# Performance work log

Hardware: AMD Instinct MI355X
Metric: run time of the kernel (lower is better)

Reference implementation:

```python
import jax, jax.numpy as jnp
import numpy as np

N, E, G = 50000, 800000, 128          # nodes, edges, graphs
L, T, F = 4, 4, 20                    # conv layers, towers, per-tower width
D = T * F                             # 80 = hidden dim
EDGE_DIM = 16
AVG_DEG_LOG = float(np.log(17.0))     # avg_deg['log'] for avg in-degree ~16
EPS_STD = 1e-5
EPS_BN = 1e-5


def setup_inputs() -> dict:
    ks = iter(jax.random.split(jax.random.key(0), 32))
    rn = lambda *s: jax.random.normal(next(ks), s, jnp.float32) * 0.1
    return dict(
        x=jax.random.randint(next(ks), (N, 9), 0, 16),
        edge_index=jax.random.randint(next(ks), (2, E), 0, N),
        batch=jnp.sort(jax.random.randint(next(ks), (N,), 0, G)),
        edge_attr=rn(E, EDGE_DIM),
        atom_emb=rn(9, 16, D),
        edge_w=rn(L, EDGE_DIM, F), edge_b=jnp.zeros((L, F), jnp.float32),
        pre_w1=rn(L, T, 3 * F, F), pre_b1=jnp.zeros((L, T, F), jnp.float32),
        pre_w2=rn(L, T, F, F), pre_b2=jnp.zeros((L, T, F), jnp.float32),
        post_w1=rn(L, T, 13 * F, F), post_b1=jnp.zeros((L, T, F), jnp.float32),
        post_w2=rn(L, T, F, F), post_b2=jnp.zeros((L, T, F), jnp.float32),
        lin_w=rn(L, D, D), lin_b=jnp.zeros((L, D), jnp.float32),
        bn_g=jnp.ones((L, D), jnp.float32), bn_b=jnp.zeros((L, D), jnp.float32),
        mlp_w1=rn(D, 40), mlp_b1=jnp.zeros(40, jnp.float32),
        mlp_w2=rn(40, 20), mlp_b2=jnp.zeros(20, jnp.float32),
        mlp_w3=rn(20, 1), mlp_b3=jnp.zeros(1, jnp.float32),
    )


def _net(x, edge_index, batch, edge_attr, atom_emb, edge_w, edge_b, pre_w1,
         pre_b1, pre_w2, pre_b2, post_w1, post_b1, post_w2, post_b2, lin_w,
         lin_b, bn_g, bn_b, mlp_w1, mlp_b1, mlp_w2, mlp_b2, mlp_w3, mlp_b3):
    src, dst = edge_index[0], edge_index[1]
    # AtomEncoder: sum of 9 categorical embeddings -> [N, D]
    h = atom_emb[jnp.arange(9)[None, :], x].sum(1)
    deg_raw = jax.ops.segment_sum(jnp.ones((E,), jnp.float32), dst, N)
    deg = jnp.clip(deg_raw, 1.0)
    has_edge = (deg_raw > 0)[:, None, None]
    d3 = deg[:, None, None]
    logd = jnp.log(deg + 1.0)[:, None, None]
    for l in range(L):  # 4 PNAConv + BN + ReLU + residual (dropout off / eval)
        xt = h.reshape(N, T, F)
        ea = edge_attr @ edge_w[l] + edge_b[l]                      # [E, F]
        # message: concat(x_i, x_j, edge) -> per-tower pre MLP
        m = jnp.concatenate([xt[dst], xt[src],
                             jnp.broadcast_to(ea[:, None, :], (E, T, F))], -1)
        m = jax.nn.relu(jnp.einsum('eti,tio->eto', m, pre_w1[l]) + pre_b1[l])
        m = jnp.einsum('eti,tio->eto', m, pre_w2[l]) + pre_b2[l]    # [E,T,F]
        # multi-aggregator scatter-reduce
        mean = jax.ops.segment_sum(m, dst, N) / d3
        msq = jax.ops.segment_sum(m * m, dst, N) / d3
        std = jnp.sqrt(jax.nn.relu(msq - mean * mean) + EPS_STD)
        mn = jnp.where(has_edge, jax.ops.segment_min(m, dst, N), 0.0)
        mx = jnp.where(has_edge, jax.ops.segment_max(m, dst, N), 0.0)
        agg = jnp.concatenate([mean, mn, mx, std], -1)              # [N,T,4F]
        # degree scalers: identity, amplification, attenuation
        out = jnp.concatenate([agg, agg * (logd / AVG_DEG_LOG),
                               agg * (AVG_DEG_LOG / logd)], -1)     # [N,T,12F]
        out = jnp.concatenate([xt, out], -1)                        # [N,T,13F]
        out = jax.nn.relu(jnp.einsum('nti,tio->nto', out, post_w1[l]) + post_b1[l])
        out = jnp.einsum('nti,tio->nto', out, post_w2[l]) + post_b2[l]
        out = out.reshape(N, D) @ lin_w[l] + lin_b[l]
        # BatchNorm over nodes (batch statistics)
        mu = out.mean(0)
        var = jnp.mean((out - mu) ** 2, axis=0)
        out = (out - mu) * (bn_g[l] / jnp.sqrt(var + EPS_BN)) + bn_b[l]
        h = jax.nn.relu(out) + h
    # global mean pool over graphs + readout MLP
    cnt = jnp.clip(jax.ops.segment_sum(jnp.ones((N,), jnp.float32), batch, G), 1.0)
    g = jax.ops.segment_sum(h, batch, G) / cnt[:, None]
    g = jax.nn.relu(g @ mlp_w1 + mlp_b1)
    g = jax.nn.relu(g @ mlp_w2 + mlp_b2)
    return g @ mlp_w3 + mlp_b3                                      # [G, 1]


def reference(x, edge_index, batch, edge_attr, atom_emb, edge_w, edge_b, pre_w1,
              pre_b1, pre_w2, pre_b2, post_w1, post_b1, post_w2, post_b2, lin_w,
              lin_b, bn_g, bn_b, mlp_w1, mlp_b1, mlp_w2, mlp_b2, mlp_w3, mlp_b3):
    return _net(x, edge_index, batch, edge_attr, atom_emb, edge_w, edge_b, pre_w1,
                pre_b1, pre_w2, pre_b2, post_w1, post_b1, post_w2, post_b2,
                lin_w, lin_b, bn_g, bn_b, mlp_w1, mlp_b1, mlp_w2, mlp_b2,
                mlp_w3, mlp_b3)
```

## Files before the change

### kernel.cpp

```cpp
#include <hip/hip_runtime.h>
#include <hip/hip_bf16.h>

#define NN 50000
#define EE 800000
#define GG 128
#define LL 4
#define TT 4
#define FF 20
#define DD 80
#define SCAN_B ((NN + 1023) / 1024)
static constexpr float AVG_LOG = 2.8332133440562162f;

__device__ __forceinline__ float bf2f(unsigned short u) {
  return __uint_as_float((unsigned)u << 16);
}
__device__ __forceinline__ unsigned short f2bf(float f) {
  __hip_bfloat16 b = __float2bfloat16(f);
  return *(unsigned short*)&b;
}

__global__ __launch_bounds__(256) void k_h(const int* __restrict__ x,
                                           const float* __restrict__ atom_emb,
                                           float* __restrict__ h) {
  int idx = blockIdx.x * 256 + threadIdx.x;
  if (idx >= NN * DD) return;
  int n = idx / DD, d = idx - n * DD;
  const int* xr = x + n * 9;
  float acc = 0.f;
#pragma unroll
  for (int i = 0; i < 9; ++i) {
    int v = xr[i];
    acc += atom_emb[(i * 16 + v) * DD + d];
  }
  h[idx] = acc;
}

__global__ __launch_bounds__(256) void k_deg(const int* __restrict__ ei, int* __restrict__ cnt) {
  int e = blockIdx.x * 256 + threadIdx.x;
  if (e >= EE) return;
  atomicAdd(&cnt[ei[EE + e]], 1);
}

__global__ __launch_bounds__(1024) void k_scan_sum(const int* __restrict__ cnt, int* __restrict__ bsum) {
  __shared__ int red[1024];
  int tid = threadIdx.x;
  int i = blockIdx.x * 1024 + tid;
  red[tid] = (i < NN) ? cnt[i] : 0;
  __syncthreads();
  for (int off = 512; off > 0; off >>= 1) {
    if (tid < off) red[tid] += red[tid + off];
    __syncthreads();
  }
  if (tid == 0) bsum[blockIdx.x] = red[0];
}

__global__ void k_scan_top(const int* __restrict__ bsum, int* __restrict__ boff,
                           int* __restrict__ row_ptr) {
  if (threadIdx.x == 0 && blockIdx.x == 0) {
    int acc = 0;
    for (int b = 0; b < SCAN_B; ++b) { boff[b] = acc; acc += bsum[b]; }
    row_ptr[NN] = acc;
  }
}

__global__ __launch_bounds__(1024) void k_scan_apply(const int* __restrict__ cnt,
                                                     const int* __restrict__ boff,
                                                     int* __restrict__ row_ptr,
                                                     int* __restrict__ cursor) {
  __shared__ int sm[1024];
  int tid = threadIdx.x;
  int i = blockIdx.x * 1024 + tid;
  int v = (i < NN) ? cnt[i] : 0;
  sm[tid] = v;
  __syncthreads();
  for (int off = 1; off < 1024; off <<= 1) {
    int t = (tid >= off) ? sm[tid - off] : 0;
    __syncthreads();
    sm[tid] += t;
    __syncthreads();
  }
  int excl = boff[blockIdx.x] + sm[tid] - v;
  if (i < NN) { row_ptr[i] = excl; cursor[i] = excl; }
}

__global__ __launch_bounds__(256) void k_csrfill(const int* __restrict__ ei,
                                                 int* __restrict__ cursor,
                                                 int2* __restrict__ csr2,
                                                 int* __restrict__ csr_dst) {
  int e = blockIdx.x * 256 + threadIdx.x;
  if (e >= EE) return;
  int dst = ei[EE + e];
  int slot = atomicAdd(&cursor[dst], 1);
  csr2[slot] = make_int2(ei[e], e);
  csr_dst[slot] = dst;
}

__global__ __launch_bounds__(256) void k_nodeparams(const int* __restrict__ cnt,
                                                    float* __restrict__ inv_deg,
                                                    float* __restrict__ s1a,
                                                    float* __restrict__ s2a) {
  int n = blockIdx.x * 256 + threadIdx.x;
  if (n >= NN) return;
  int c = cnt[n];
  float deg = (c > 0) ? (float)c : 1.0f;
  inv_deg[n] = 1.0f / deg;
  float logd = logf(deg + 1.0f);
  s1a[n] = logd / AVG_LOG;
  s2a[n] = AVG_LOG / logd;
}

__global__ __launch_bounds__(64) void k_wcomb(const float* __restrict__ edge_w,
                                              const float* __restrict__ edge_b,
                                              const float* __restrict__ pre_w1,
                                              const float* __restrict__ pre_b1,
                                              float* __restrict__ wc,
                                              float* __restrict__ biasc, int l) {
  int t = blockIdx.x;
  int wt = l * TT + t;
  const float* W1 = pre_w1 + (size_t)wt * 1200;
  const float* ew = edge_w + (size_t)l * 16 * FF;
  const float* eb = edge_b + (size_t)l * FF;
  int j = threadIdx.x;
  if (j >= FF) return;
  for (int i = 0; i < 16; ++i) {
    float acc = 0.f;
#pragma unroll
    for (int f = 0; f < FF; ++f) acc = fmaf(ew[i * FF + f], W1[(40 + f) * FF + j], acc);
    wc[(t * 16 + i) * FF + j] = acc;
  }
  float b = pre_b1[wt * FF + j];
#pragma unroll
  for (int f = 0; f < FF; ++f) b = fmaf(eb[f], W1[(40 + f) * FF + j], b);
  biasc[t * FF + j] = b;
}

__global__ __launch_bounds__(256) void k_prenode(
    const float* __restrict__ h, const float* __restrict__ pre_w1,
    const float* __restrict__ biasc,
    unsigned short* __restrict__ predD, unsigned short* __restrict__ predS, int l) {
  int tid = threadIdx.x;
  int t = tid >> 6, lane = tid & 63;
  int n = blockIdx.x * 64 + lane;
  if (n >= NN) return;
  int wt_u = __builtin_amdgcn_readfirstlane(l * TT + t);
  const float* W1 = pre_w1 + (size_t)wt_u * 1200;
  const float* bc = biasc + t * FF;
  float xt[FF];
  {
    const float4* pp = (const float4*)(h + (size_t)n * DD + t * FF);
#pragma unroll
    for (int i = 0; i < 5; ++i) { float4 v = pp[i]; xt[i*4]=v.x; xt[i*4+1]=v.y; xt[i*4+2]=v.z; xt[i*4+3]=v.w; }
  }
  float d[FF], s[FF];
#pragma unroll
  for (int j = 0; j < FF; ++j) { d[j] = bc[j]; s[j] = 0.f; }
#pragma unroll
  for (int i = 0; i < FF; ++i) {
    float a = xt[i];
#pragma unroll
    for (int j = 0; j < FF; ++j) {
      d[j] = fmaf(a, W1[i * FF + j], d[j]);
      s[j] = fmaf(a, W1[(FF + i) * FF + j], s[j]);
    }
  }
  ushort4* pd = (ushort4*)(predD + (size_t)n * DD + t * FF);
  ushort4* ps = (ushort4*)(predS + (size_t)n * DD + t * FF);
#pragma unroll
  for (int i = 0; i < 5; ++i) {
    pd[i] = make_ushort4(f2bf(d[i*4]), f2bf(d[i*4+1]), f2bf(d[i*4+2]), f2bf(d[i*4+3]));
    ps[i] = make_ushort4(f2bf(s[i*4]), f2bf(s[i*4+1]), f2bf(s[i*4+2]), f2bf(s[i*4+3]));
  }
}

__global__ __launch_bounds__(256, 4) void k_pre(
    const unsigned short* __restrict__ predD, const unsigned short* __restrict__ predS,
    const float* __restrict__ edge_attr,
    const int2* __restrict__ csr2, const int* __restrict__ csr_dst,
    const int* __restrict__ row_ptr,
    const float* __restrict__ wc,
    const float* __restrict__ pre_w2, const float* __restrict__ pre_b2,
    __hip_bfloat16* __restrict__ m, int l, int n0, int n1, int capSlots) {
  int tid = threadIdx.x;
  int t = tid >> 6;
  int lane = tid & 63;
  int wt_u = __builtin_amdgcn_readfirstlane(l * TT + t);
  int t_u  = __builtin_amdgcn_readfirstlane(t);
  const float* W2 = pre_w2 + (size_t)wt_u * 400;
  const float* b2 = pre_b2 + (size_t)wt_u * FF;
  const float* Wc = wc + (size_t)t_u * 16 * FF;

  int sl = blockIdx.x * 64 + lane;
  int base = row_ptr[n0], end = row_ptr[n1];
  if (sl >= capSlots || base + sl >= end) return;
  int p = base + sl;
  int2 se = csr2[p];
  int dst = csr_dst[p];

  float m1[FF];
  {
    const ushort4* pp = (const ushort4*)(predD + (size_t)dst * DD + t * FF);
    const ushort4* qq = (const ushort4*)(predS + (size_t)se.x * DD + t * FF);
#pragma unroll
    for (int i = 0; i < 5; ++i) {
      ushort4 u = pp[i];
      ushort4 v = qq[i];
      m1[i*4+0] = bf2f(u.x) + bf2f(v.x);
      m1[i*4+1] = bf2f(u.y) + bf2f(v.y);
      m1[i*4+2] = bf2f(u.z) + bf2f(v.z);
      m1[i*4+3] = bf2f(u.w) + bf2f(v.w);
    }
  }
  {
    float a[16];
    const float4* ap = (const float4*)(edge_attr + (size_t)se.y * 16);
#pragma unroll
    for (int i = 0; i < 4; ++i) { float4 v = ap[i]; a[i*4]=v.x; a[i*4+1]=v.y; a[i*4+2]=v.z; a[i*4+3]=v.w; }
#pragma unroll
    for (int i = 0; i < 16; ++i) {
      float av = a[i];
#pragma unroll
      for (int j = 0; j < FF; ++j) m1[j] = fmaf(av, Wc[i * FF + j], m1[j]);
    }
  }
#pragma unroll
  for (int j = 0; j < FF; ++j) m1[j] = fmaxf(m1[j], 0.f);
  float m2[FF];
#pragma unroll
  for (int j = 0; j < FF; ++j) m2[j] = b2[j];
#pragma unroll
  for (int i = 0; i < FF; ++i) {
    float a = m1[i];
#pragma unroll
    for (int j = 0; j < FF; ++j) m2[j] = fmaf(a, W2[i * FF + j], m2[j]);
  }
  __hip_bfloat16* mrow = m + (size_t)t * FF * capSlots + sl;
#pragma unroll
  for (int j = 0; j < FF; ++j) mrow[(size_t)j * capSlots] = __float2bfloat16(m2[j]);
}

__global__ __launch_bounds__(320) void k_agg(
    const __hip_bfloat16* __restrict__ m,
    const int* __restrict__ row_ptr,
    const float* __restrict__ inv_deg,
    unsigned short* __restrict__ aggbuf, int n0, int n1, int capSlots) {
  int tid = threadIdx.x;
  int t = blockIdx.x & 3, tile = blockIdx.x >> 2;
  int ni = tid / FF, j = tid - ni * FF;
  int n = n0 + tile * 16 + ni;
  if (n >= n1) return;
  int base = row_ptr[n0];
  int beg = row_ptr[n], end = row_ptr[n + 1];
  float inv = inv_deg[n];
  int s0 = beg - base, s1c = end - base;
  if (s0 < 0) s0 = 0;
  if (s1c > capSlots) s1c = capSlots;
  float sum = 0.f, sq = 0.f, mnv = 3.4e38f, mxv = -3.4e38f;
  const unsigned short* mrow = (const unsigned short*)(m + (size_t)(t * FF + j) * capSlots);
  int p = s0;
  for (; p < s1c && (p & 3); ++p) {
    float v = bf2f(mrow[p]);
    sum += v; sq += v * v; mnv = fminf(mnv, v); mxv = fmaxf(mxv, v);
  }
  for (; p + 4 <= s1c; p += 4) {
    ushort4 u = *(const ushort4*)(mrow + p);
    float v0 = bf2f(u.x), v1 = bf2f(u.y), v2 = bf2f(u.z), v3 = bf2f(u.w);
    sum += (v0 + v1) + (v2 + v3);
    sq  += (v0 * v0 + v1 * v1) + (v2 * v2 + v3 * v3);
    mnv = fminf(mnv, fminf(fminf(v0, v1), fminf(v2, v3)));
    mxv = fmaxf(mxv, fmaxf(fmaxf(v0, v1), fmaxf(v2, v3)));
  }
  for (; p < s1c; ++p) {
    float v = bf2f(mrow[p]);
    sum += v; sq += v * v; mnv = fminf(mnv, v); mxv = fmaxf(mxv, v);
  }
  float mu = sum * inv;
  float var = sq * inv - mu * mu;
  float sd = sqrtf(fmaxf(var, 0.f) + 1e-5f);
  if (end <= beg) { mnv = 0.f; mxv = 0.f; }
  unsigned short* ab = aggbuf + ((size_t)(n - n0) * 4 + t) * 80;
  ab[j]      = f2bf(mu);
  ab[20 + j] = f2bf(mnv);
  ab[40 + j] = f2bf(mxv);
  ab[60 + j] = f2bf(sd);
}

__global__ __launch_bounds__(256) void k_post2(
    const float* __restrict__ h, const unsigned short* __restrict__ aggbuf,
    const float* __restrict__ s1a, const float* __restrict__ s2a,
    const float* __restrict__ post_w1, const float* __restrict__ post_b1,
    const float* __restrict__ post_w2, const float* __restrict__ post_b2,
    float* __restrict__ out2, int l, int n0, int n1) {
  int tid = threadIdx.x;
  int t = tid >> 6, lane = tid & 63;
  int wt_u = __builtin_amdgcn_readfirstlane(l * TT + t);
  const float* Q1 = post_w1 + (size_t)wt_u * 5200;
  const float* Q2 = post_w2 + (size_t)wt_u * 400;
  const float* B1 = post_b1 + (size_t)wt_u * FF;
  const float* B2 = post_b2 + (size_t)wt_u * FF;
  int n = n0 + blockIdx.x * 64 + lane;
  if (n >= n1) return;
  float c1 = s1a[n], c2 = s2a[n];
  float o1[FF];
#pragma unroll
  for (int j = 0; j < FF; ++j) o1[j] = B1[j];
  const float* hrow = h + (size_t)n * DD + t * FF;
  for (int i = 0; i < FF; ++i) {
    float a = hrow[i];
#pragma unroll
    for (int j = 0; j < FF; ++j) o1[j] = fmaf(a, Q1[i * FF + j], o1[j]);
  }
  const unsigned short* ab = aggbuf + ((size_t)(n - n0) * 4 + t) * 80;
  for (int i = 0; i < 80; ++i) {
    float a0 = bf2f(ab[i]);
    float a1 = a0 * c1, a2 = a0 * c2;
    int r = FF + i;
#pragma unroll
    for (int j = 0; j < FF; ++j) o1[j] = fmaf(a0, Q1[r * FF + j], o1[j]);
#pragma unroll
    for (int j = 0; j < FF; ++j) o1[j] = fmaf(a1, Q1[(r + 80) * FF + j], o1[j]);
#pragma unroll
    for (int j = 0; j < FF; ++j) o1[j] = fmaf(a2, Q1[(r + 160) * FF + j], o1[j]);
  }
#pragma unroll
  for (int j = 0; j < FF; ++j) o1[j] = fmaxf(o1[j], 0.f);
  float o2[FF];
#pragma unroll
  for (int j = 0; j < FF; ++j) o2[j] = B2[j];
#pragma unroll
  for (int i = 0; i < FF; ++i) {
    float a = o1[i];
#pragma unroll
    for (int j = 0; j < FF; ++j) o2[j] = fmaf(a, Q2[i * FF + j], o2[j]);
  }
  float4* op = (float4*)(out2 + (size_t)n * DD + t * FF);
#pragma unroll
  for (int i = 0; i < 5; ++i) op[i] = make_float4(o2[i*4], o2[i*4+1], o2[i*4+2], o2[i*4+3]);
}

__global__ __launch_bounds__(320) void k_lin(const float* __restrict__ out2,
                                             const float* __restrict__ lin_w,
                                             const float* __restrict__ lin_b,
                                             float* __restrict__ outl,
                                             float* __restrict__ colsum, int l) {
  __shared__ float Wl[DD * DD];
  __shared__ float rowbuf[4 * DD];
  __shared__ float red[320];
  int tid = threadIdx.x;
  for (int i = tid; i < DD * DD; i += 320) Wl[i] = lin_w[(size_t)l * DD * DD + i];
  __syncthreads();
  int nl = tid / DD, d = tid - nl * DD;
  float bias = lin_b[l * DD + d];
  float bsum = 0.f, bsq = 0.f;
  for (int base = blockIdx.x * 4; base < NN; base += gridDim.x * 4) {
    int gi = base * DD + tid;
    rowbuf[tid] = (gi < NN * DD) ? out2[gi] : 0.f;
    __syncthreads();
    int n = base + nl;
    if (n < NN) {
      float acc = bias;
#pragma unroll
      for (int i = 0; i < DD; ++i) acc = fmaf(rowbuf[nl * DD + i], Wl[i * DD + d], acc);
      outl[(size_t)n * DD + d] = acc;
      bsum += acc; bsq += acc * acc;
    }
    __syncthreads();
  }
// ... 62 lines not shown
  int nl = tid / DD, d = tid - nl * DD;
  int start = gstart[g], c = gcnt[g];
  float acc = 0.f;
  for (int r = start + nl; r < start + c; r += 4) acc += h[(size_t)r * DD + d];
  red[tid] = acc;
  __syncthreads();
  if (tid < DD) {
    float s = red[tid] + red[tid + DD] + red[tid + 2 * DD] + red[tid + 3 * DD];
    float cf = (c > 0) ? (float)c : 1.0f;
    gbuf[g * DD + tid] = s / cf;
  }
}

__global__ __launch_bounds__(64) void k_mlp(const float* __restrict__ gbuf,
                                            const float* __restrict__ w1, const float* __restrict__ b1,
                                            const float* __restrict__ w2, const float* __restrict__ b2,
                                            const float* __restrict__ w3, const float* __restrict__ b3,
                                            float* __restrict__ out) {
  __shared__ float row[DD];
  __shared__ float t1[40];
  __shared__ float t2[20];
  int g = blockIdx.x, tid = threadIdx.x;
  for (int i = tid; i < DD; i += 64) row[i] = gbuf[g * DD + i];
  __syncthreads();
  if (tid < 40) {
    float acc = b1[tid];
#pragma unroll
    for (int i = 0; i < DD; ++i) acc = fmaf(row[i], w1[i * 40 + tid], acc);
    t1[tid] = fmaxf(acc, 0.f);
  }
  __syncthreads();
  if (tid < 20) {
    float acc = b2[tid];
#pragma unroll
    for (int i = 0; i < 40; ++i) acc = fmaf(t1[i], w2[i * 20 + tid], acc);
    t2[tid] = fmaxf(acc, 0.f);
  }
  __syncthreads();
  if (tid == 0) {
    float acc = b3[0];
#pragma unroll
    for (int i = 0; i < 20; ++i) acc = fmaf(t2[i], w3[i], acc);
    out[g] = acc;
  }
}

extern "C" void kernel_launch(void* const* d_in, const int* in_sizes, int n_in,
                              void* d_out, int out_size, void* d_ws, size_t ws_size,
                              hipStream_t stream) {
  const int*   x         = (const int*)d_in[0];
  const int*   ei        = (const int*)d_in[1];
  const int*   batch     = (const int*)d_in[2];
  const float* edge_attr = (const float*)d_in[3];
  const float* atom_emb  = (const float*)d_in[4];
  const float* edge_w    = (const float*)d_in[5];
  const float* edge_b    = (const float*)d_in[6];
  const float* pre_w1    = (const float*)d_in[7];
  const float* pre_b1    = (const float*)d_in[8];
  const float* pre_w2    = (const float*)d_in[9];
  const float* pre_b2    = (const float*)d_in[10];
  const float* post_w1   = (const float*)d_in[11];
  const float* post_b1   = (const float*)d_in[12];
  const float* post_w2   = (const float*)d_in[13];
  const float* post_b2   = (const float*)d_in[14];
  const float* lin_w     = (const float*)d_in[15];
  const float* lin_b     = (const float*)d_in[16];
  const float* bn_g      = (const float*)d_in[17];
  const float* bn_b      = (const float*)d_in[18];
  const float* mlp_w1    = (const float*)d_in[19];
  const float* mlp_b1    = (const float*)d_in[20];
  const float* mlp_w2    = (const float*)d_in[21];
  const float* mlp_b2    = (const float*)d_in[22];
  const float* mlp_w3    = (const float*)d_in[23];
  const float* mlp_b3    = (const float*)d_in[24];
  float* out = (float*)d_out;

  char* ws = (char*)d_ws;
  size_t off = 0;
  auto alloc = [&](size_t bytes) -> void* {
    void* p = ws + off;
    off += (bytes + 15) & ~(size_t)15;
    return p;
  };
  float* h       = (float*)alloc((size_t)NN * DD * 4);
  float* out2    = (float*)alloc((size_t)NN * DD * 4);
  unsigned short* predD = (unsigned short*)alloc((size_t)NN * DD * 2);
  unsigned short* predS = (unsigned short*)alloc((size_t)NN * DD * 2);
  int2*  csr2    = (int2*)alloc((size_t)EE * 8);
  int*   csr_dst = (int*)alloc((size_t)EE * 4);
  int*   row_ptr = (int*)alloc((size_t)(NN + 1) * 4);
  int*   cnt     = (int*)alloc((size_t)NN * 4);
  int*   cursor  = (int*)alloc((size_t)NN * 4);
  float* inv_deg = (float*)alloc((size_t)NN * 4);
  float* s1a     = (float*)alloc((size_t)NN * 4);
  float* s2a     = (float*)alloc((size_t)NN * 4);
  float* colsum  = (float*)alloc(2 * DD * 4);
  float* bnsc    = (float*)alloc(2 * DD * 4);
  float* gbuf    = (float*)alloc((size_t)GG * DD * 4);
  float* wc      = (float*)alloc((size_t)TT * 16 * FF * 4);
  float* biasc   = (float*)alloc((size_t)TT * FF * 4);
  int*   bsum    = (int*)alloc((size_t)SCAN_B * 4);
  int*   boff    = (int*)alloc((size_t)SCAN_B * 4);
  int*   gcnt    = (int*)alloc((size_t)GG * 4);
  int*   gstart  = (int*)alloc((size_t)(GG + 1) * 4);
  (void)in_sizes; (void)n_in; (void)out_size;

  size_t rest = (ws_size > off) ? (ws_size - off) : 0;
  static const int cands[] = {1, 2, 4, 5, 8, 10, 20, 25, 40, 50};
  int c = -1, capSlots = 0, nodesPer = 0;
  size_t aggBytes = 0;
  for (int ci = 0; ci < 10; ++ci) {
    int cc = cands[ci];
    int np = (NN + cc - 1) / cc;
    size_t ab = ((size_t)np * 4 * 80 * 2 + 63) & ~(size_t)63;
    int slots = EE / cc + 25000; if (slots > EE) slots = EE;
    slots = (slots + 63) & ~63;
    size_t mb = (size_t)slots * DD * 2;
    if (ab + mb <= rest && ab + mb >= (size_t)NN * DD * 4) {
      c = cc; capSlots = slots; nodesPer = np; aggBytes = ab;
      break;
    }
  }
  if (c < 0) {
    c = 50; nodesPer = (NN + c - 1) / c;
    aggBytes = ((size_t)nodesPer * 4 * 80 * 2 + 63) & ~(size_t)63;
    size_t mb = (rest > aggBytes) ? rest - aggBytes : 0;
    capSlots = (int)(mb / (DD * 2)) & ~63;
  }
  unsigned short* aggbuf = (unsigned short*)(ws + off);
  __hip_bfloat16* mbuf = (__hip_bfloat16*)(ws + off + aggBytes);
  float* outl = (float*)(ws + off);

  hipMemsetAsync(cnt, 0, (size_t)NN * 4, stream);
  k_h<<<(NN * DD + 255) / 256, 256, 0, stream>>>(x, atom_emb, h);
  k_deg<<<(EE + 255) / 256, 256, 0, stream>>>(ei, cnt);
  k_scan_sum<<<SCAN_B, 1024, 0, stream>>>(cnt, bsum);
  k_scan_top<<<1, 64, 0, stream>>>(bsum, boff, row_ptr);
  k_scan_apply<<<SCAN_B, 1024, 0, stream>>>(cnt, boff, row_ptr, cursor);
  k_csrfill<<<(EE + 255) / 256, 256, 0, stream>>>(ei, cursor, csr2, csr_dst);
  k_nodeparams<<<(NN + 255) / 256, 256, 0, stream>>>(cnt, inv_deg, s1a, s2a);

  for (int l = 0; l < LL; ++l) {
    k_wcomb<<<TT, 64, 0, stream>>>(edge_w, edge_b, pre_w1, pre_b1, wc, biasc, l);
    k_prenode<<<(NN + 63) / 64, 256, 0, stream>>>(h, pre_w1, biasc, predD, predS, l);
    for (int ck = 0; ck < c; ++ck) {
      int n0 = ck * nodesPer;
      int n1 = n0 + nodesPer; if (n1 > NN) n1 = NN;
      if (n0 >= n1) continue;
      int preBlocks = (capSlots + 63) / 64;
      k_pre<<<preBlocks, 256, 0, stream>>>(predD, predS, edge_attr, csr2, csr_dst, row_ptr,
          wc, pre_w2, pre_b2, mbuf, l, n0, n1, capSlots);
      int aggBlocks = ((n1 - n0 + 15) / 16) * 4;
      k_agg<<<aggBlocks, 320, 0, stream>>>(mbuf, row_ptr, inv_deg, aggbuf, n0, n1, capSlots);
      int p2Blocks = (n1 - n0 + 63) / 64;
      k_post2<<<p2Blocks, 256, 0, stream>>>(h, aggbuf, s1a, s2a,
          post_w1, post_b1, post_w2, post_b2, out2, l, n0, n1);
    }
    hipMemsetAsync(colsum, 0, 2 * DD * 4, stream);
    k_lin<<<512, 320, 0, stream>>>(out2, lin_w, lin_b, outl, colsum, l);
    k_bnfinal<<<1, 128, 0, stream>>>(colsum, bn_g, bn_b, bnsc, l);
    k_bnapply<<<(NN * DD + 255) / 256, 256, 0, stream>>>(outl, bnsc, h);
  }

  hipMemsetAsync(gcnt, 0, (size_t)GG * 4, stream);
  k_gcnt<<<(NN + 255) / 256, 256, 0, stream>>>(batch, gcnt);
  k_gstart<<<1, 64, 0, stream>>>(gcnt, gstart);
  k_gmean<<<GG, 320, 0, stream>>>(h, gstart, gcnt, gbuf);
  k_mlp<<<GG, 64, 0, stream>>>(gbuf, mlp_w1, mlp_b1, mlp_w2, mlp_b2, mlp_w3, mlp_b3, out);
}
```

Baseline: 1.653 ms.

## Fuse edge message MLP with per-node aggregation using degree-sorted node order

Replaces the per-edge message kernel, which wrote bf16 messages to a large buffer, and the separate aggregation kernel with one node-centric kernel. Each thread walks its node's CSR edge list, computes messages in registers and accumulates sum, sum of squares, min and max directly. Nodes are bucketed by in-degree so threads in a wavefront have similar loop trip counts. The destination projection is computed once per node instead of being stored and gathered per edge, and the chunking logic over workspace and the csr_dst array are removed. In exchange, per-thread serial loops lengthen and register pressure rises (launch bounds change to 256,2). There is also a prefetch read of csr2[p+1] that can run one element past the end of the array for the last edge.

```diff
diff --git a/kernel.cpp b/kernel.cpp
--- a/kernel.cpp
+++ b/kernel.cpp
@@ -9,6 +9,7 @@
 #define FF 20
 #define DD 80
 #define SCAN_B ((NN + 1023) / 1024)
+#define DEGB 64
 static constexpr float AVG_LOG = 2.8332133440562162f;
 
 __device__ __forceinline__ float bf2f(unsigned short u) {
@@ -85,14 +86,12 @@
 
 __global__ __launch_bounds__(256) void k_csrfill(const int* __restrict__ ei,
                                                  int* __restrict__ cursor,
-                                                 int2* __restrict__ csr2,
-                                                 int* __restrict__ csr_dst) {
+                                                 int2* __restrict__ csr2) {
   int e = blockIdx.x * 256 + threadIdx.x;
   if (e >= EE) return;
   int dst = ei[EE + e];
   int slot = atomicAdd(&cursor[dst], 1);
   csr2[slot] = make_int2(ei[e], e);
-  csr_dst[slot] = dst;
 }
 
 __global__ __launch_bounds__(256) void k_nodeparams(const int* __restrict__ cnt,
@@ -107,6 +106,32 @@
   float logd = logf(deg + 1.0f);
   s1a[n] = logd / AVG_LOG;
   s2a[n] = AVG_LOG / logd;
+}
+
+__global__ __launch_bounds__(256) void k_deghist(const int* __restrict__ cnt, int* __restrict__ hist) {
+  int n = blockIdx.x * 256 + threadIdx.x;
+  if (n >= NN) return;
+  int b = cnt[n];
+  if (b > DEGB - 1) b = DEGB - 1;
+  atomicAdd(&hist[b], 1);
+}
+
+__global__ void k_degoff(const int* __restrict__ hist, int* __restrict__ cur) {
+  if (threadIdx.x == 0 && blockIdx.x == 0) {
+    int acc = 0;
+    for (int b = DEGB - 1; b >= 0; --b) { cur[b] = acc; acc += hist[b]; }
+  }
+}
+
+__global__ __launch_bounds__(256) void k_degscatter(const int* __restrict__ cnt,
+                                                    int* __restrict__ cur,
+                                                    int* __restrict__ nodeperm) {
+  int n = blockIdx.x * 256 + threadIdx.x;
+  if (n >= NN) return;
+  int b = cnt[n];
+  if (b > DEGB - 1) b = DEGB - 1;
+  int pos = atomicAdd(&cur[b], 1);
+  nodeperm[pos] = n;
 }
 
 __global__ __launch_bounds__(64) void k_wcomb(const float* __restrict__ edge_w,
@@ -134,154 +159,158 @@
   biasc[t * FF + j] = b;
 }
 
-__global__ __launch_bounds__(256) void k_prenode(
+__global__ __launch_bounds__(256) void k_presrc(
     const float* __restrict__ h, const float* __restrict__ pre_w1,
-    const float* __restrict__ biasc,
-    unsigned short* __restrict__ predD, unsigned short* __restrict__ predS, int l) {
+    unsigned short* __restrict__ predS, int l) {
   int tid = threadIdx.x;
   int t = tid >> 6, lane = tid & 63;
   int n = blockIdx.x * 64 + lane;
   if (n >= NN) return;
   int wt_u = __builtin_amdgcn_readfirstlane(l * TT + t);
   const float* W1 = pre_w1 + (size_t)wt_u * 1200;
-  const float* bc = biasc + t * FF;
   float xt[FF];
   {
     const float4* pp = (const float4*)(h + (size_t)n * DD + t * FF);
 #pragma unroll
     for (int i = 0; i < 5; ++i) { float4 v = pp[i]; xt[i*4]=v.x; xt[i*4+1]=v.y; xt[i*4+2]=v.z; xt[i*4+3]=v.w; }
   }
-  float d[FF], s[FF];
-#pragma unroll
-  for (int j = 0; j < FF; ++j) { d[j] = bc[j]; s[j] = 0.f; }
+  float s[FF];
+#pragma unroll
+  for (int j = 0; j < FF; ++j) s[j] = 0.f;
 #pragma unroll
   for (int i = 0; i < FF; ++i) {
     float a = xt[i];
 #pragma unroll
-    for (int j = 0; j < FF; ++j) {
-      d[j] = fmaf(a, W1[i * FF + j], d[j]);
-      s[j] = fmaf(a, W1[(FF + i) * FF + j], s[j]);
-    }
-  }
-  ushort4* pd = (ushort4*)(predD + (size_t)n * DD + t * FF);
+    for (int j = 0; j < FF; ++j) s[j] = fmaf(a, W1[(FF + i) * FF + j], s[j]);
+  }
   ushort4* ps = (ushort4*)(predS + (size_t)n * DD + t * FF);
 #pragma unroll
-  for (int i = 0; i < 5; ++i) {
-    pd[i] = make_ushort4(f2bf(d[i*4]), f2bf(d[i*4+1]), f2bf(d[i*4+2]), f2bf(d[i*4+3]));
+  for (int i = 0; i < 5; ++i)
     ps[i] = make_ushort4(f2bf(s[i*4]), f2bf(s[i*4+1]), f2bf(s[i*4+2]), f2bf(s[i*4+3]));
-  }
-}
-
-__global__ __launch_bounds__(256, 4) void k_pre(
-    const unsigned short* __restrict__ predD, const unsigned short* __restrict__ predS,
+}
+
+__global__ __launch_bounds__(256, 2) void k_preagg(
+    const float* __restrict__ h,
+    const unsigned short* __restrict__ predS,
     const float* __restrict__ edge_attr,
-    const int2* __restrict__ csr2, const int* __restrict__ csr_dst,
+    const int2* __restrict__ csr2,
     const int* __restrict__ row_ptr,
+    const int* __restrict__ nodeperm,
+    const float* __restrict__ inv_deg,
+    const float* __restrict__ pre_w1,
     const float* __restrict__ wc,
-    const float* __restrict__ pre_w2, const float* __restrict__ pre_b2,
-    __hip_bfloat16* __restrict__ m, int l, int n0, int n1, int capSlots) {
+    const float* __restrict__ biasc,
+    const float* __restrict__ pre_w2,
+    const float* __restrict__ pre_b2,
+    unsigned short* __restrict__ aggbuf,
+    int l) {
   int tid = threadIdx.x;
-  int t = tid >> 6;
-  int lane = tid & 63;
+  int t = tid >> 6, lane = tid & 63;
   int wt_u = __builtin_amdgcn_readfirstlane(l * TT + t);
   int t_u  = __builtin_amdgcn_readfirstlane(t);
+  const float* W1 = pre_w1 + (size_t)wt_u * 1200;
   const float* W2 = pre_w2 + (size_t)wt_u * 400;
   const float* b2 = pre_b2 + (size_t)wt_u * FF;
   const float* Wc = wc + (size_t)t_u * 16 * FF;
-
-  int sl = blockIdx.x * 64 + lane;
-  int base = row_ptr[n0], end = row_ptr[n1];
-  if (sl >= capSlots || base + sl >= end) return;
-  int p = base + sl;
-  int2 se = csr2[p];
-  int dst = csr_dst[p];
-
-  float m1[FF];
+  const float* bc = biasc + (size_t)t_u * FF;
+
+  int idx = blockIdx.x * 64 + lane;
+  if (idx >= NN) return;
+  int n = nodeperm[idx];
+
+  float dD[FF];
+#pragma unroll
+  for (int j = 0; j < FF; ++j) dD[j] = bc[j];
   {
-    const ushort4* pp = (const ushort4*)(predD + (size_t)dst * DD + t * FF);
-    const ushort4* qq = (const ushort4*)(predS + (size_t)se.x * DD + t * FF);
+    float xt[FF];
+    const float4* pp = (const float4*)(h + (size_t)n * DD + t * FF);
+#pragma unroll
+    for (int i = 0; i < 5; ++i) { float4 v = pp[i]; xt[i*4]=v.x; xt[i*4+1]=v.y; xt[i*4+2]=v.z; xt[i*4+3]=v.w; }
+#pragma unroll
+    for (int i = 0; i < FF; ++i) {
+      float a = xt[i];
+#pragma unroll
+      for (int j = 0; j < FF; ++j) dD[j] = fmaf(a, W1[i * FF + j], dD[j]);
+    }
+  }
+
+  int beg = row_ptr[n], end = row_ptr[n + 1];
+  float sum[FF], sq[FF], mnv[FF], mxv[FF];
+#pragma unroll
+  for (int j = 0; j < FF; ++j) { sum[j] = 0.f; sq[j] = 0.f; mnv[j] = 3.4e38f; mxv[j] = -3.4e38f; }
+
+  int2 se = (beg < end) ? csr2[beg] : make_int2(0, 0);
+  for (int p = beg; p < end; ++p) {
+    int2 se_n = csr2[p + 1];
+    ushort4 uu[5];
+    {
+      const ushort4* qq = (const ushort4*)(predS + (size_t)se.x * DD + t * FF);
+#pragma unroll
+      for (int i = 0; i < 5; ++i) uu[i] = qq[i];
+    }
+    float a[16];
+    {
+      const float4* ap = (const float4*)(edge_attr + (size_t)se.y * 16);
+#pragma unroll
+      for (int i = 0; i < 4; ++i) { float4 v = ap[i]; a[i*4]=v.x; a[i*4+1]=v.y; a[i*4+2]=v.z; a[i*4+3]=v.w; }
+    }
+    float m1[FF];
 #pragma unroll
     for (int i = 0; i < 5; ++i) {
-      ushort4 u = pp[i];
-      ushort4 v = qq[i];
-      m1[i*4+0] = bf2f(u.x) + bf2f(v.x);
-      m1[i*4+1] = bf2f(u.y) + bf2f(v.y);
-      m1[i*4+2] = bf2f(u.z) + bf2f(v.z);
-      m1[i*4+3] = bf2f(u.w) + bf2f(v.w);
-    }
-  }
-  {
-    float a[16];
-    const float4* ap = (const float4*)(edge_attr + (size_t)se.y * 16);
-#pragma unroll
-    for (int i = 0; i < 4; ++i) { float4 v = ap[i]; a[i*4]=v.x; a[i*4+1]=v.y; a[i*4+2]=v.z; a[i*4+3]=v.w; }
+      m1[i*4+0] = dD[i*4+0] + bf2f(uu[i].x);
+      m1[i*4+1] = dD[i*4+1] + bf2f(uu[i].y);
+      m1[i*4+2] = dD[i*4+2] + bf2f(uu[i].z);
+      m1[i*4+3] = dD[i*4+3] + bf2f(uu[i].w);
+    }
 #pragma unroll
     for (int i = 0; i < 16; ++i) {
       float av = a[i];
 #pragma unroll
       for (int j = 0; j < FF; ++j) m1[j] = fmaf(av, Wc[i * FF + j], m1[j]);
     }
-  }
-#pragma unroll
-  for (int j = 0; j < FF; ++j) m1[j] = fmaxf(m1[j], 0.f);
-  float m2[FF];
-#pragma unroll
-  for (int j = 0; j < FF; ++j) m2[j] = b2[j];
-#pragma unroll
-  for (int i = 0; i < FF; ++i) {
-    float a = m1[i];
-#pragma unroll
-    for (int j = 0; j < FF; ++j) m2[j] = fmaf(a, W2[i * FF + j], m2[j]);
-  }
-  __hip_bfloat16* mrow = m + (size_t)t * FF * capSlots + sl;
-#pragma unroll
-  for (int j = 0; j < FF; ++j) mrow[(size_t)j * capSlots] = __float2bfloat16(m2[j]);
-}
-
-__global__ __launch_bounds__(320) void k_agg(
-    const __hip_bfloat16* __restrict__ m,
-    const int* __restrict__ row_ptr,
-    const float* __restrict__ inv_deg,
-    unsigned short* __restrict__ aggbuf, int n0, int n1, int capSlots) {
-  int tid = threadIdx.x;
-  int t = blockIdx.x & 3, tile = blockIdx.x >> 2;
-  int ni = tid / FF, j = tid - ni * FF;
-  int n = n0 + tile * 16 + ni;
-  if (n >= n1) return;
-  int base = row_ptr[n0];
-  int beg = row_ptr[n], end = row_ptr[n + 1];
+#pragma unroll
+    for (int j = 0; j < FF; ++j) m1[j] = fmaxf(m1[j], 0.f);
+    float m2[FF];
+#pragma unroll
+    for (int j = 0; j < FF; ++j) m2[j] = b2[j];
+#pragma unroll
+    for (int i = 0; i < FF; ++i) {
+      float av = m1[i];
+#pragma unroll
+      for (int j = 0; j < FF; ++j) m2[j] = fmaf(av, W2[i * FF + j], m2[j]);
+    }
+#pragma unroll
+    for (int j = 0; j < FF; ++j) {
+      float v = m2[j];
+      sum[j] += v;
+      sq[j] = fmaf(v, v, sq[j]);
+      mnv[j] = fminf(mnv[j], v);
+      mxv[j] = fmaxf(mxv[j], v);
+    }
+    se = se_n;
+  }
+
   float inv = inv_deg[n];
-  int s0 = beg - base, s1c = end - base;
-  if (s0 < 0) s0 = 0;
-  if (s1c > capSlots) s1c = capSlots;
-  float sum = 0.f, sq = 0.f, mnv = 3.4e38f, mxv = -3.4e38f;
-  const unsigned short* mrow = (const unsigned short*)(m + (size_t)(t * FF + j) * capSlots);
-  int p = s0;
-  for (; p < s1c && (p & 3); ++p) {
-    float v = bf2f(mrow[p]);
-    sum += v; sq += v * v; mnv = fminf(mnv, v); mxv = fmaxf(mxv, v);
-  }
-  for (; p + 4 <= s1c; p += 4) {
-    ushort4 u = *(const ushort4*)(mrow + p);
-    float v0 = bf2f(u.x), v1 = bf2f(u.y), v2 = bf2f(u.z), v3 = bf2f(u.w);
-    sum += (v0 + v1) + (v2 + v3);
-    sq  += (v0 * v0 + v1 * v1) + (v2 * v2 + v3 * v3);
-    mnv = fminf(mnv, fminf(fminf(v0, v1), fminf(v2, v3)));
-    mxv = fmaxf(mxv, fmaxf(fmaxf(v0, v1), fmaxf(v2, v3)));
-  }
-  for (; p < s1c; ++p) {
-    float v = bf2f(mrow[p]);
-    sum += v; sq += v * v; mnv = fminf(mnv, v); mxv = fmaxf(mxv, v);
-  }
-  float mu = sum * inv;
-  float var = sq * inv - mu * mu;
-  float sd = sqrtf(fmaxf(var, 0.f) + 1e-5f);
-  if (end <= beg) { mnv = 0.f; mxv = 0.f; }
-  unsigned short* ab = aggbuf + ((size_t)(n - n0) * 4 + t) * 80;
-  ab[j]      = f2bf(mu);
-  ab[20 + j] = f2bf(mnv);
-  ab[40 + j] = f2bf(mxv);
-  ab[60 + j] = f2bf(sd);
+  float mu[FF], sd[FF];
+#pragma unroll
+  for (int j = 0; j < FF; ++j) {
+    float m = sum[j] * inv;
+    float var = sq[j] * inv - m * m;
+    mu[j] = m;
+    sd[j] = sqrtf(fmaxf(var, 0.f) + 1e-5f);
+  }
+  if (end <= beg) {
+#pragma unroll
+    for (int j = 0; j < FF; ++j) { mnv[j] = 0.f; mxv[j] = 0.f; }
+  }
+  ushort4* ab4 = (ushort4*)(aggbuf + ((size_t)n * 4 + t) * 80);
+#pragma unroll
+  for (int i = 0; i < 5; ++i) {
+    ab4[i]      = make_ushort4(f2bf(mu[i*4]),  f2bf(mu[i*4+1]),  f2bf(mu[i*4+2]),  f2bf(mu[i*4+3]));
+    ab4[5 + i]  = make_ushort4(f2bf(mnv[i*4]), f2bf(mnv[i*4+1]), f2bf(mnv[i*4+2]), f2bf(mnv[i*4+3]));
+    ab4[10 + i] = make_ushort4(f2bf(mxv[i*4]), f2bf(mxv[i*4+1]), f2bf(mxv[i*4+2]), f2bf(mxv[i*4+3]));
+    ab4[15 + i] = make_ushort4(f2bf(sd[i*4]),  f2bf(sd[i*4+1]),  f2bf(sd[i*4+2]),  f2bf(sd[i*4+3]));
+  }
 }
 
 __global__ __launch_bounds__(256) void k_post2(
@@ -510,80 +539,53 @@
     off += (bytes + 15) & ~(size_t)15;
     return p;
   };
-  float* h       = (float*)alloc((size_t)NN * DD * 4);
-  float* out2    = (float*)alloc((size_t)NN * DD * 4);
-  unsigned short* predD = (unsigned short*)alloc((size_t)NN * DD * 2);
+  float* h        = (float*)alloc((size_t)NN * DD * 4);
+  float* out2     = (float*)alloc((size_t)NN * DD * 4);
   unsigned short* predS = (unsigned short*)alloc((size_t)NN * DD * 2);
-  int2*  csr2    = (int2*)alloc((size_t)EE * 8);
-  int*   csr_dst = (int*)alloc((size_t)EE * 4);
-  int*   row_ptr = (int*)alloc((size_t)(NN + 1) * 4);
-  int*   cnt     = (int*)alloc((size_t)NN * 4);
-  int*   cursor  = (int*)alloc((size_t)NN * 4);
-  float* inv_deg = (float*)alloc((size_t)NN * 4);
-  float* s1a     = (float*)alloc((size_t)NN * 4);
-  float* s2a     = (float*)alloc((size_t)NN * 4);
-  float* colsum  = (float*)alloc(2 * DD * 4);
-  float* bnsc    = (float*)alloc(2 * DD * 4);
-  float* gbuf    = (float*)alloc((size_t)GG * DD * 4);
-  float* wc      = (float*)alloc((size_t)TT * 16 * FF * 4);
-  float* biasc   = (float*)alloc((size_t)TT * FF * 4);
-  int*   bsum    = (int*)alloc((size_t)SCAN_B * 4);
-  int*   boff    = (int*)alloc((size_t)SCAN_B * 4);
-  int*   gcnt    = (int*)alloc((size_t)GG * 4);
-  int*   gstart  = (int*)alloc((size_t)(GG + 1) * 4);
-  (void)in_sizes; (void)n_in; (void)out_size;
-
-  size_t rest = (ws_size > off) ? (ws_size - off) : 0;
-  static const int cands[] = {1, 2, 4, 5, 8, 10, 20, 25, 40, 50};
-  int c = -1, capSlots = 0, nodesPer = 0;
-  size_t aggBytes = 0;
-  for (int ci = 0; ci < 10; ++ci) {
-    int cc = cands[ci];
-    int np = (NN + cc - 1) / cc;
-    size_t ab = ((size_t)np * 4 * 80 * 2 + 63) & ~(size_t)63;
-    int slots = EE / cc + 25000; if (slots > EE) slots = EE;
-    slots = (slots + 63) & ~63;
-    size_t mb = (size_t)slots * DD * 2;
-    if (ab + mb <= rest && ab + mb >= (size_t)NN * DD * 4) {
-      c = cc; capSlots = slots; nodesPer = np; aggBytes = ab;
-      break;
-    }
-  }
-  if (c < 0) {
-    c = 50; nodesPer = (NN + c - 1) / c;
-    aggBytes = ((size_t)nodesPer * 4 * 80 * 2 + 63) & ~(size_t)63;
-    size_t mb = (rest > aggBytes) ? rest - aggBytes : 0;
-    capSlots = (int)(mb / (DD * 2)) & ~63;
-  }
-  unsigned short* aggbuf = (unsigned short*)(ws + off);
-  __hip_bfloat16* mbuf = (__hip_bfloat16*)(ws + off + aggBytes);
-  float* outl = (float*)(ws + off);
+  int2*  csr2     = (int2*)alloc((size_t)EE * 8);
+  int*   row_ptr  = (int*)alloc((size_t)(NN + 1) * 4);
+  int*   cnt      = (int*)alloc((size_t)NN * 4);
+  int*   cursor   = (int*)alloc((size_t)NN * 4);
+  int*   nodeperm = (int*)alloc((size_t)NN * 4);
+  float* inv_deg  = (float*)alloc((size_t)NN * 4);
+  float* s1a      = (float*)alloc((size_t)NN * 4);
+  float* s2a      = (float*)alloc((size_t)NN * 4);
+  float* colsum   = (float*)alloc(2 * DD * 4);
+  float* bnsc     = (float*)alloc(2 * DD * 4);
+  float* gbuf     = (float*)alloc((size_t)GG * DD * 4);
+  float* wc       = (float*)alloc((size_t)TT * 16 * FF * 4);
+  float* biasc    = (float*)alloc((size_t)TT * FF * 4);
+  int*   bsum     = (int*)alloc((size_t)SCAN_B * 4);
+  int*   boff     = (int*)alloc((size_t)SCAN_B * 4);
+  int*   gcnt     = (int*)alloc((size_t)GG * 4);
+  int*   gstart   = (int*)alloc((size_t)(GG + 1) * 4);
+  int*   hist     = (int*)alloc((size_t)DEGB * 4);
+  int*   histcur  = (int*)alloc((size_t)DEGB * 4);
+  unsigned short* aggbuf = (unsigned short*)alloc((size_t)NN * 4 * 80 * 2);
+  float* outl = (float*)aggbuf;
+  (void)in_sizes; (void)n_in; (void)out_size; (void)ws_size;
 
   hipMemsetAsync(cnt, 0, (size_t)NN * 4, stream);
+  hipMemsetAsync(hist, 0, (size_t)DEGB * 4, stream);
   k_h<<<(NN * DD + 255) / 256, 256, 0, stream>>>(x, atom_emb, h);
   k_deg<<<(EE + 255) / 256, 256, 0, stream>>>(ei, cnt);
   k_scan_sum<<<SCAN_B, 1024, 0, stream>>>(cnt, bsum);
   k_scan_top<<<1, 64, 0, stream>>>(bsum, boff, row_ptr);
   k_scan_apply<<<SCAN_B, 1024, 0, stream>>>(cnt, boff, row_ptr, cursor);
-  k_csrfill<<<(EE + 255) / 256, 256, 0, stream>>>(ei, cursor, csr2, csr_dst);
+  k_csrfill<<<(EE + 255) / 256, 256, 0, stream>>>(ei, cursor, csr2);
   k_nodeparams<<<(NN + 255) / 256, 256, 0, stream>>>(cnt, inv_deg, s1a, s2a);
-
+  k_deghist<<<(NN + 255) / 256, 256, 0, stream>>>(cnt, hist);
+  k_degoff<<<1, 64, 0, stream>>>(hist, histcur);
+  k_degscatter<<<(NN + 255) / 256, 256, 0, stream>>>(cnt, histcur, nodeperm);
+
+  int nodeBlocks = (NN + 63) / 64;
   for (int l = 0; l < LL; ++l) {
     k_wcomb<<<TT, 64, 0, stream>>>(edge_w, edge_b, pre_w1, pre_b1, wc, biasc, l);
-    k_prenode<<<(NN + 63) / 64, 256, 0, stream>>>(h, pre_w1, biasc, predD, predS, l);
-    for (int ck = 0; ck < c; ++ck) {
-      int n0 = ck * nodesPer;
-      int n1 = n0 + nodesPer; if (n1 > NN) n1 = NN;
-      if (n0 >= n1) continue;
-      int preBlocks = (capSlots + 63) / 64;
-      k_pre<<<preBlocks, 256, 0, stream>>>(predD, predS, edge_attr, csr2, csr_dst, row_ptr,
-          wc, pre_w2, pre_b2, mbuf, l, n0, n1, capSlots);
-      int aggBlocks = ((n1 - n0 + 15) / 16) * 4;
-      k_agg<<<aggBlocks, 320, 0, stream>>>(mbuf, row_ptr, inv_deg, aggbuf, n0, n1, capSlots);
-      int p2Blocks = (n1 - n0 + 63) / 64;
-      k_post2<<<p2Blocks, 256, 0, stream>>>(h, aggbuf, s1a, s2a,
-          post_w1, post_b1, post_w2, post_b2, out2, l, n0, n1);
-    }
+    k_presrc<<<nodeBlocks, 256, 0, stream>>>(h, pre_w1, predS, l);
+    k_preagg<<<nodeBlocks, 256, 0, stream>>>(h, predS, edge_attr, csr2, row_ptr,
+        nodeperm, inv_deg, pre_w1, wc, biasc, pre_w2, pre_b2, aggbuf, l);
+    k_post2<<<nodeBlocks, 256, 0, stream>>>(h, aggbuf, s1a, s2a,
+        post_w1, post_b1, post_w2, post_b2, out2, l, 0, NN);
     hipMemsetAsync(colsum, 0, 2 * DD * 4, stream);
     k_lin<<<512, 320, 0, stream>>>(out2, lin_w, lin_b, outl, colsum, l);
     k_bnfinal<<<1, 128, 0, stream>>>(colsum, bn_g, bn_b, bnsc, l);
```

Result: slower. 2.222 ms (+34.4%).

## Use packed fp16 dot2 for edge MLP and store messages as half2 pairs

Applied to the files above, without the earlier changes.

The per-edge pre-MLP (edge-attr projection and second layer) now uses packed fp16 dot2 instructions, with weights pre-packed into half2 by the weight-combine kernel. Messages are stored as interleaved half2 pairs, so the aggregation kernel reads two features per 32-bit load, handles 32 nodes per block, and writes packed bf16 pairs. This halves the FMA instruction count in the edge kernel and widens the aggregation loads. The cost is reduced precision (fp16 with round-toward-zero conversions) and a possible overflow risk in fp16 range.

```diff
diff --git a/kernel.cpp b/kernel.cpp
--- a/kernel.cpp
+++ b/kernel.cpp
@@ -11,12 +11,41 @@
 #define SCAN_B ((NN + 1023) / 1024)
 static constexpr float AVG_LOG = 2.8332133440562162f;
 
+typedef __fp16 half2v __attribute__((ext_vector_type(2)));
+
 __device__ __forceinline__ float bf2f(unsigned short u) {
   return __uint_as_float((unsigned)u << 16);
 }
 __device__ __forceinline__ unsigned short f2bf(float f) {
   __hip_bfloat16 b = __float2bfloat16(f);
   return *(unsigned short*)&b;
+}
+__device__ __forceinline__ half2v pkrtz(float a, float b) {
+#if __has_builtin(__builtin_amdgcn_cvt_pkrtz)
+  return __builtin_amdgcn_cvt_pkrtz(a, b);
+#else
+  half2v h; h.x = (__fp16)a; h.y = (__fp16)b; return h;
+#endif
+}
+__device__ __forceinline__ float fdot2(half2v a, half2v b, float c) {
+#if __has_builtin(__builtin_amdgcn_fdot2)
+  return __builtin_amdgcn_fdot2(a, b, c, false);
+#else
+  return fmaf((float)a.x, (float)b.x, fmaf((float)a.y, (float)b.y, c));
+#endif
+}
+__device__ __forceinline__ half2v u2h2(unsigned int u) {
+  return __builtin_bit_cast(half2v, u);
+}
+__device__ __forceinline__ unsigned int h22u(half2v h) {
+  return __builtin_bit_cast(unsigned int, h);
+}
+__device__ __forceinline__ unsigned int packh2_rne(float a, float b) {
+  half2v h; h.x = (__fp16)a; h.y = (__fp16)b;
+  return h22u(h);
+}
+__device__ __forceinline__ unsigned int pack_bf16(float a, float b) {
+  return (unsigned int)f2bf(a) | ((unsigned int)f2bf(b) << 16);
 }
 
 __global__ __launch_bounds__(256) void k_h(const int* __restrict__ x,
@@ -113,21 +142,31 @@
                                               const float* __restrict__ edge_b,
                                               const float* __restrict__ pre_w1,
                                               const float* __restrict__ pre_b1,
-                                              float* __restrict__ wc,
+                                              const float* __restrict__ pre_w2,
+                                              unsigned int* __restrict__ wcpk,
+                                              unsigned int* __restrict__ w2pk,
                                               float* __restrict__ biasc, int l) {
   int t = blockIdx.x;
   int wt = l * TT + t;
   const float* W1 = pre_w1 + (size_t)wt * 1200;
+  const float* W2 = pre_w2 + (size_t)wt * 400;
   const float* ew = edge_w + (size_t)l * 16 * FF;
   const float* eb = edge_b + (size_t)l * FF;
   int j = threadIdx.x;
   if (j >= FF) return;
+  float col[16];
   for (int i = 0; i < 16; ++i) {
     float acc = 0.f;
 #pragma unroll
     for (int f = 0; f < FF; ++f) acc = fmaf(ew[i * FF + f], W1[(40 + f) * FF + j], acc);
-    wc[(t * 16 + i) * FF + j] = acc;
-  }
+    col[i] = acc;
+  }
+#pragma unroll
+  for (int i2 = 0; i2 < 8; ++i2)
+    wcpk[((size_t)t * FF + j) * 8 + i2] = packh2_rne(col[2 * i2], col[2 * i2 + 1]);
+#pragma unroll
+  for (int i2 = 0; i2 < 10; ++i2)
+    w2pk[((size_t)t * FF + j) * 10 + i2] = packh2_rne(W2[(2 * i2) * FF + j], W2[(2 * i2 + 1) * FF + j]);
   float b = pre_b1[wt * FF + j];
 #pragma unroll
   for (int f = 0; f < FF; ++f) b = fmaf(eb[f], W1[(40 + f) * FF + j], b);
@@ -177,17 +216,18 @@
     const float* __restrict__ edge_attr,
     const int2* __restrict__ csr2, const int* __restrict__ csr_dst,
     const int* __restrict__ row_ptr,
-    const float* __restrict__ wc,
-    const float* __restrict__ pre_w2, const float* __restrict__ pre_b2,
-    __hip_bfloat16* __restrict__ m, int l, int n0, int n1, int capSlots) {
+    const unsigned int* __restrict__ wcpk,
+    const unsigned int* __restrict__ w2pk,
+    const float* __restrict__ pre_b2,
+    unsigned int* __restrict__ m, int l, int n0, int n1, int capSlots) {
   int tid = threadIdx.x;
   int t = tid >> 6;
   int lane = tid & 63;
   int wt_u = __builtin_amdgcn_readfirstlane(l * TT + t);
   int t_u  = __builtin_amdgcn_readfirstlane(t);
-  const float* W2 = pre_w2 + (size_t)wt_u * 400;
+  const unsigned int* Wcp = wcpk + (size_t)t_u * FF * 8;
+  const unsigned int* W2p = w2pk + (size_t)t_u * FF * 10;
   const float* b2 = pre_b2 + (size_t)wt_u * FF;
-  const float* Wc = wc + (size_t)t_u * 16 * FF;
 
   int sl = blockIdx.x * 64 + lane;
   int base = row_ptr[n0], end = row_ptr[n1];
@@ -210,43 +250,50 @@
       m1[i*4+3] = bf2f(u.w) + bf2f(v.w);
     }
   }
+  half2v eap[8];
   {
-    float a[16];
     const float4* ap = (const float4*)(edge_attr + (size_t)se.y * 16);
 #pragma unroll
-    for (int i = 0; i < 4; ++i) { float4 v = ap[i]; a[i*4]=v.x; a[i*4+1]=v.y; a[i*4+2]=v.z; a[i*4+3]=v.w; }
-#pragma unroll
-    for (int i = 0; i < 16; ++i) {
-      float av = a[i];
-#pragma unroll
-      for (int j = 0; j < FF; ++j) m1[j] = fmaf(av, Wc[i * FF + j], m1[j]);
+    for (int i = 0; i < 4; ++i) {
+      float4 v = ap[i];
+      eap[2*i]   = pkrtz(v.x, v.y);
+      eap[2*i+1] = pkrtz(v.z, v.w);
     }
   }
 #pragma unroll
-  for (int j = 0; j < FF; ++j) m1[j] = fmaxf(m1[j], 0.f);
+  for (int j = 0; j < FF; ++j) {
+    float c = m1[j];
+#pragma unroll
+    for (int i2 = 0; i2 < 8; ++i2) c = fdot2(eap[i2], u2h2(Wcp[j * 8 + i2]), c);
+    m1[j] = c;
+  }
+  half2v mp[10];
+#pragma unroll
+  for (int pr = 0; pr < 10; ++pr)
+    mp[pr] = pkrtz(fmaxf(m1[2*pr], 0.f), fmaxf(m1[2*pr+1], 0.f));
   float m2[FF];
 #pragma unroll
-  for (int j = 0; j < FF; ++j) m2[j] = b2[j];
-#pragma unroll
-  for (int i = 0; i < FF; ++i) {
-    float a = m1[i];
-#pragma unroll
-    for (int j = 0; j < FF; ++j) m2[j] = fmaf(a, W2[i * FF + j], m2[j]);
-  }
-  __hip_bfloat16* mrow = m + (size_t)t * FF * capSlots + sl;
-#pragma unroll
-  for (int j = 0; j < FF; ++j) mrow[(size_t)j * capSlots] = __float2bfloat16(m2[j]);
+  for (int j = 0; j < FF; ++j) {
+    float c = b2[j];
+#pragma unroll
+    for (int i2 = 0; i2 < 10; ++i2) c = fdot2(mp[i2], u2h2(W2p[j * 10 + i2]), c);
+    m2[j] = c;
+  }
+  unsigned int* mrow = m + (size_t)t * 10 * capSlots + sl;
+#pragma unroll
+  for (int pr = 0; pr < 10; ++pr)
+    mrow[(size_t)pr * capSlots] = h22u(pkrtz(m2[2*pr], m2[2*pr+1]));
 }
 
 __global__ __launch_bounds__(320) void k_agg(
-    const __hip_bfloat16* __restrict__ m,
+    const unsigned int* __restrict__ m,
     const int* __restrict__ row_ptr,
     const float* __restrict__ inv_deg,
     unsigned short* __restrict__ aggbuf, int n0, int n1, int capSlots) {
   int tid = threadIdx.x;
   int t = blockIdx.x & 3, tile = blockIdx.x >> 2;
-  int ni = tid / FF, j = tid - ni * FF;
-  int n = n0 + tile * 16 + ni;
+  int ni = tid / 10, pr = tid - ni * 10;
+  int n = n0 + tile * 32 + ni;
   if (n >= n1) return;
   int base = row_ptr[n0];
   int beg = row_ptr[n], end = row_ptr[n + 1];
@@ -254,34 +301,42 @@
   int s0 = beg - base, s1c = end - base;
   if (s0 < 0) s0 = 0;
   if (s1c > capSlots) s1c = capSlots;
-  float sum = 0.f, sq = 0.f, mnv = 3.4e38f, mxv = -3.4e38f;
-  const unsigned short* mrow = (const unsigned short*)(m + (size_t)(t * FF + j) * capSlots);
+  float sum0 = 0.f, sum1 = 0.f, sq0 = 0.f, sq1 = 0.f;
+  float mn0 = 3.4e38f, mn1 = 3.4e38f, mx0 = -3.4e38f, mx1 = -3.4e38f;
+  const unsigned int* mrow = m + (size_t)(t * 10 + pr) * capSlots;
   int p = s0;
   for (; p < s1c && (p & 3); ++p) {
-    float v = bf2f(mrow[p]);
-    sum += v; sq += v * v; mnv = fminf(mnv, v); mxv = fmaxf(mxv, v);
+    half2v h = u2h2(mrow[p]);
+    float v0 = (float)h.x, v1 = (float)h.y;
+    sum0 += v0; sq0 = fmaf(v0, v0, sq0); mn0 = fminf(mn0, v0); mx0 = fmaxf(mx0, v0);
+    sum1 += v1; sq1 = fmaf(v1, v1, sq1); mn1 = fminf(mn1, v1); mx1 = fmaxf(mx1, v1);
   }
   for (; p + 4 <= s1c; p += 4) {
-    ushort4 u = *(const ushort4*)(mrow + p);
-    float v0 = bf2f(u.x), v1 = bf2f(u.y), v2 = bf2f(u.z), v3 = bf2f(u.w);
-    sum += (v0 + v1) + (v2 + v3);
-    sq  += (v0 * v0 + v1 * v1) + (v2 * v2 + v3 * v3);
-    mnv = fminf(mnv, fminf(fminf(v0, v1), fminf(v2, v3)));
-    mxv = fmaxf(mxv, fmaxf(fmaxf(v0, v1), fmaxf(v2, v3)));
+    uint4 q = *(const uint4*)(mrow + p);
+#pragma unroll
+    for (int k = 0; k < 4; ++k) {
+      unsigned int u = (k == 0) ? q.x : (k == 1) ? q.y : (k == 2) ? q.z : q.w;
+      half2v h = u2h2(u);
+      float v0 = (float)h.x, v1 = (float)h.y;
+      sum0 += v0; sq0 = fmaf(v0, v0, sq0); mn0 = fminf(mn0, v0); mx0 = fmaxf(mx0, v0);
+      sum1 += v1; sq1 = fmaf(v1, v1, sq1); mn1 = fminf(mn1, v1); mx1 = fmaxf(mx1, v1);
+    }
   }
   for (; p < s1c; ++p) {
-    float v = bf2f(mrow[p]);
-    sum += v; sq += v * v; mnv = fminf(mnv, v); mxv = fmaxf(mxv, v);
-  }
-  float mu = sum * inv;
-  float var = sq * inv - mu * mu;
-  float sd = sqrtf(fmaxf(var, 0.f) + 1e-5f);
-  if (end <= beg) { mnv = 0.f; mxv = 0.f; }
+    half2v h = u2h2(mrow[p]);
+    float v0 = (float)h.x, v1 = (float)h.y;
+    sum0 += v0; sq0 = fmaf(v0, v0, sq0); mn0 = fminf(mn0, v0); mx0 = fmaxf(mx0, v0);
+    sum1 += v1; sq1 = fmaf(v1, v1, sq1); mn1 = fminf(mn1, v1); mx1 = fmaxf(mx1, v1);
+  }
+  float mu0 = sum0 * inv, mu1 = sum1 * inv;
+  float sd0 = sqrtf(fmaxf(sq0 * inv - mu0 * mu0, 0.f) + 1e-5f);
+  float sd1 = sqrtf(fmaxf(sq1 * inv - mu1 * mu1, 0.f) + 1e-5f);
+  if (end <= beg) { mn0 = 0.f; mn1 = 0.f; mx0 = 0.f; mx1 = 0.f; }
   unsigned short* ab = aggbuf + ((size_t)(n - n0) * 4 + t) * 80;
-  ab[j]      = f2bf(mu);
-  ab[20 + j] = f2bf(mnv);
-  ab[40 + j] = f2bf(mxv);
-  ab[60 + j] = f2bf(sd);
+  ((unsigned int*)(ab))[pr]      = pack_bf16(mu0, mu1);
+  ((unsigned int*)(ab + 20))[pr] = pack_bf16(mn0, mn1);
+  ((unsigned int*)(ab + 40))[pr] = pack_bf16(mx0, mx1);
+  ((unsigned int*)(ab + 60))[pr] = pack_bf16(sd0, sd1);
 }
 
 __global__ __launch_bounds__(256) void k_post2(
@@ -525,7 +580,8 @@
   float* colsum  = (float*)alloc(2 * DD * 4);
   float* bnsc    = (float*)alloc(2 * DD * 4);
   float* gbuf    = (float*)alloc((size_t)GG * DD * 4);
-  float* wc      = (float*)alloc((size_t)TT * 16 * FF * 4);
+  unsigned int* wcpk  = (unsigned int*)alloc((size_t)TT * FF * 8 * 4);
+  unsigned int* w2pk  = (unsigned int*)alloc((size_t)TT * FF * 10 * 4);
   float* biasc   = (float*)alloc((size_t)TT * FF * 4);
   int*   bsum    = (int*)alloc((size_t)SCAN_B * 4);
   int*   boff    = (int*)alloc((size_t)SCAN_B * 4);
@@ -556,7 +612,7 @@
     capSlots = (int)(mb / (DD * 2)) & ~63;
   }
   unsigned short* aggbuf = (unsigned short*)(ws + off);
-  __hip_bfloat16* mbuf = (__hip_bfloat16*)(ws + off + aggBytes);
+  unsigned int* mbuf = (unsigned int*)(ws + off + aggBytes);
   float* outl = (float*)(ws + off);
 
   hipMemsetAsync(cnt, 0, (size_t)NN * 4, stream);
@@ -569,7 +625,7 @@
   k_nodeparams<<<(NN + 255) / 256, 256, 0, stream>>>(cnt, inv_deg, s1a, s2a);
 
   for (int l = 0; l < LL; ++l) {
-    k_wcomb<<<TT, 64, 0, stream>>>(edge_w, edge_b, pre_w1, pre_b1, wc, biasc, l);
+    k_wcomb<<<TT, 64, 0, stream>>>(edge_w, edge_b, pre_w1, pre_b1, pre_w2, wcpk, w2pk, biasc, l);
     k_prenode<<<(NN + 63) / 64, 256, 0, stream>>>(h, pre_w1, biasc, predD, predS, l);
     for (int ck = 0; ck < c; ++ck) {
       int n0 = ck * nodesPer;
@@ -577,8 +633,8 @@
       if (n0 >= n1) continue;
       int preBlocks = (capSlots + 63) / 64;
       k_pre<<<preBlocks, 256, 0, stream>>>(predD, predS, edge_attr, csr2, csr_dst, row_ptr,
-          wc, pre_w2, pre_b2, mbuf, l, n0, n1, capSlots);
-      int aggBlocks = ((n1 - n0 + 15) / 16) * 4;
+          wcpk, w2pk, pre_b2, mbuf, l, n0, n1, capSlots);
+      int aggBlocks = ((n1 - n0 + 31) / 32) * 4;
       k_agg<<<aggBlocks, 320, 0, stream>>>(mbuf, row_ptr, inv_deg, aggbuf, n0, n1, capSlots);
       int p2Blocks = (n1 - n0 + 63) / 64;
       k_post2<<<p2Blocks, 256, 0, stream>>>(h, aggbuf, s1a, s2a,
```

Result: faster. 1.550 ms (-6.2%).
